# Kernel tuning notes

Hardware: AMD Instinct MI355X
Metric: run time of the kernel (lower is better)

The kernel has to match this reference:

```python
import jax, jax.numpy as jnp
import numpy as np
from math import factorial


def _su2_cg(j1, j2, j3, m1, m2, m3):
    # Complex SU(2) Clebsch-Gordan coefficient <j1 m1; j2 m2 | j3 m3> (Condon-Shortley),
    # same formula as e3nn's _su2_clebsch_gordan_coeff.
    if m3 != m1 + m2:
        return 0.0
    f = factorial
    vmin = max(-j1 + j2 + m3, -j1 + m1, 0)
    vmax = min(j2 + j3 + m1, j3 - j1 + j2, j3 + m3)
    C = ((2 * j3 + 1) * f(j3 + j1 - j2) * f(j3 - j1 + j2) * f(j1 + j2 - j3) / f(j1 + j2 + j3 + 1)
         * f(j3 + m3) * f(j3 - m3) / (f(j1 - m1) * f(j1 + m1) * f(j2 - m2) * f(j2 + m2))) ** 0.5
    S = 0.0
    for v in range(vmin, vmax + 1):
        S += (-1.0) ** (v + j2 + m2) / f(v) * f(j2 + j3 + m1 - v) * f(j1 - m1 + v) / (
            f(j3 - j1 + j2 - v) * f(j3 + m3 - v) * f(v + j1 - j2 - m3))
    return C * S


def _q(l):
    # Change of basis real -> complex spherical harmonics (e3nn convention).
    q = np.zeros((2 * l + 1, 2 * l + 1), dtype=np.complex128)
    for m in range(-l, 0):
        q[l + m, l + abs(m)] = 1 / 2 ** 0.5
        q[l + m, l - abs(m)] = -1j / 2 ** 0.5
    q[l, l] = 1
    for m in range(1, l + 1):
        q[l + m, l + abs(m)] = (-1) ** m / 2 ** 0.5
        q[l + m, l - abs(m)] = 1j * (-1) ** m / 2 ** 0.5
    return (-1j) ** l * q


def _w3j(l1, l2, l3):
    # Real Wigner-3j-like invariant tensor, Frobenius norm 1 (e3nn wigner_3j).
    C = np.zeros((2 * l1 + 1, 2 * l2 + 1, 2 * l3 + 1), dtype=np.complex128)
    for m1 in range(-l1, l1 + 1):
        for m2 in range(-l2, l2 + 1):
            m3 = m1 + m2
            if -l3 <= m3 <= l3:
                C[l1 + m1, l2 + m2, l3 + m3] = _su2_cg(l1, l2, l3, m1, m2, m3)
    C = np.einsum('ij,kl,mn,ikn->jlm', _q(l1), _q(l2), np.conj(_q(l3).T), C)
    C = np.real(C)
    return C / np.linalg.norm(C)


def _cg_full():
    # 1o x 1o -> 0e + 1e + 2e. e3nn FullTensorProduct ('uuu', component norm,
    # element path norm, mul=1) gives path_weight = sqrt(2*l_out + 1) per path.
    return np.concatenate([(2 * l + 1) ** 0.5 * _w3j(1, 1, l) for l in range(3)],
                          axis=-1).astype(np.float32)  # [3, 3, 9]


def setup_inputs() -> dict:
    key = jax.random.key(0)
    N = 8388608  # 2**23 rows, ~96 MB input
    frac = jax.random.normal(key, (N, 3), dtype=jnp.float32)
    cg = jnp.asarray(_cg_full())  # [3, 3, 9] fixed Clebsch-Gordan constants
    return {"frac": frac, "cg": cg}


def reference(frac, cg):
    # SimpleTP.forward: tp(frac, frac) -> [N, 9], then sum over dim 0 -> [9].
    # Fused segment-wise CG contraction + batch reduction in one einsum.
    return jnp.einsum('ni,nj,ijk->k', frac, frac, cg)
```

## Files before the change

### kernel.cpp

```cpp
#include <hip/hip_runtime.h>


constexpr int BLK  = 256;
constexpr int GRID = 2048;

#define ACC6(x, y, z)                                              \
    do {                                                           \
        s00 = fmaf((x), (x), s00); s01 = fmaf((x), (y), s01);      \
        s02 = fmaf((x), (z), s02); s11 = fmaf((y), (y), s11);      \
        s12 = fmaf((y), (z), s12); s22 = fmaf((z), (z), s22);      \
    } while (0)

__global__ __launch_bounds__(BLK) void tp_partial(const float* __restrict__ frac,
                                                  float* __restrict__ ws,
                                                  int nrows) {
    const float4* __restrict__ f4 = reinterpret_cast<const float4*>(frac);
    const int noct   = nrows >> 3;
    const int tid    = blockIdx.x * BLK + threadIdx.x;
    const int stride = GRID * BLK;

    float s00 = 0.f, s01 = 0.f, s02 = 0.f, s11 = 0.f, s12 = 0.f, s22 = 0.f;

    #pragma unroll 2
    for (int g = tid; g < noct; g += stride) {
        const float4* __restrict__ p = f4 + 6L * g;
        float4 v0 = p[0], v1 = p[1], v2 = p[2];
        float4 v3 = p[3], v4 = p[4], v5 = p[5];
        ACC6(v0.x, v0.y, v0.z);
        ACC6(v0.w, v1.x, v1.y);
        ACC6(v1.z, v1.w, v2.x);
        ACC6(v2.y, v2.z, v2.w);
        ACC6(v3.x, v3.y, v3.z);
        ACC6(v3.w, v4.x, v4.y);
        ACC6(v4.z, v4.w, v5.x);
        ACC6(v5.y, v5.z, v5.w);
    }

    if (blockIdx.x == 0 && threadIdx.x == 0) {
        for (int r = (noct << 3); r < nrows; ++r) {
            float x = frac[3L * r + 0], y = frac[3L * r + 1], z = frac[3L * r + 2];
            ACC6(x, y, z);
        }
    }

    #pragma unroll
    for (int off = 32; off > 0; off >>= 1) {
        s00 += __shfl_down(s00, off);
        s01 += __shfl_down(s01, off);
        s02 += __shfl_down(s02, off);
        s11 += __shfl_down(s11, off);
        s12 += __shfl_down(s12, off);
        s22 += __shfl_down(s22, off);
    }

    __shared__ float red[BLK / 64][6];
    const int lane = threadIdx.x & 63;
    const int wave = threadIdx.x >> 6;
    if (lane == 0) {
        red[wave][0] = s00; red[wave][1] = s01; red[wave][2] = s02;
        red[wave][3] = s11; red[wave][4] = s12; red[wave][5] = s22;
    }
    __syncthreads();
    if (threadIdx.x < 6) {
        float v = red[0][threadIdx.x] + red[1][threadIdx.x]
                + red[2][threadIdx.x] + red[3][threadIdx.x];
        ws[threadIdx.x * GRID + blockIdx.x] = v;
    }
}

__global__ __launch_bounds__(BLK) void tp_final(const float* __restrict__ ws,
                                                const float* __restrict__ cg,
                                                float* __restrict__ out) {
    const float4* __restrict__ w4 = reinterpret_cast<const float4*>(ws);
    constexpr int Q = GRID / 4;

    float s[6];
    #pragma unroll
    for (int c = 0; c < 6; ++c) {
        float4 a = w4[c * Q + threadIdx.x];
        float4 b = w4[c * Q + threadIdx.x + BLK];
        s[c] = ((a.x + a.y) + (a.z + a.w)) + ((b.x + b.y) + (b.z + b.w));
    }

    #pragma unroll
    for (int off = 32; off > 0; off >>= 1) {
        #pragma unroll
        for (int c = 0; c < 6; ++c) s[c] += __shfl_down(s[c], off);
    }

    __shared__ float red[BLK / 64][6];
    const int lane = threadIdx.x & 63;
    const int wave = threadIdx.x >> 6;
    if (lane == 0) {
        #pragma unroll
        for (int c = 0; c < 6; ++c) red[wave][c] = s[c];
    }
    __syncthreads();

    __shared__ float M[9];
    if (threadIdx.x == 0) {
        float t[6];
        #pragma unroll
        for (int c = 0; c < 6; ++c)
            t[c] = red[0][c] + red[1][c] + red[2][c] + red[3][c];
        M[0] = t[0];  M[1] = t[1];  M[2] = t[2];
        M[3] = t[1];  M[4] = t[3];  M[5] = t[4];
        M[6] = t[2];  M[7] = t[4];  M[8] = t[5];
    }
    __syncthreads();

    if (threadIdx.x < 9) {
        const int k = threadIdx.x;
        float acc = 0.f;
        #pragma unroll
        for (int p = 0; p < 9; ++p)
            acc = fmaf(M[p], cg[p * 9 + k], acc);
        out[k] = acc;
    }
}

extern "C" void kernel_launch(void* const* d_in, const int* in_sizes, int n_in,
                              void* d_out, int out_size, void* d_ws, size_t ws_size,
                              hipStream_t stream) {
    const float* frac = (const float*)d_in[0];
    const float* cg   = (const float*)d_in[1];
    float*       out  = (float*)d_out;
    float*       ws   = (float*)d_ws;

    const int nrows = in_sizes[0] / 3;

    tp_partial<<<GRID, BLK, 0, stream>>>(frac, ws, nrows);
    tp_final<<<1, BLK, 0, stream>>>(ws, cg, out);
}
```

Baseline: 23.30 us.

## Read input as float4 quads with 2-float lookahead and phase-rotated accumulators

Each thread now reads one float4 per iteration plus the next two floats, instead of six float4s per 8-row octet. The grid is 2046 blocks, a multiple of 3, so the stride in floats is divisible by 3 and each thread's row phase (tid mod 3) stays fixed. The nine phase-relative accumulators are mapped back to the six second moments once at the end. This gives every lane a fully coalesced 16-byte load per step and fewer live registers, at the cost of redundant overlapping 8-byte loads and a padded workspace that needs extra zero writes.

```diff
diff --git a/kernel.cpp b/kernel.cpp
--- a/kernel.cpp
+++ b/kernel.cpp
@@ -2,46 +2,46 @@
 
 
 constexpr int BLK  = 256;
-constexpr int GRID = 2048;
-
-#define ACC6(x, y, z)                                              \
-    do {                                                           \
-        s00 = fmaf((x), (x), s00); s01 = fmaf((x), (y), s01);      \
-        s02 = fmaf((x), (z), s02); s11 = fmaf((y), (y), s11);      \
-        s12 = fmaf((y), (z), s12); s22 = fmaf((z), (z), s22);      \
-    } while (0)
+constexpr int GRID = 2046;
+constexpr int PG   = 2048;
 
 __global__ __launch_bounds__(BLK) void tp_partial(const float* __restrict__ frac,
                                                   float* __restrict__ ws,
-                                                  int nrows) {
+                                                  int nq) {
     const float4* __restrict__ f4 = reinterpret_cast<const float4*>(frac);
-    const int noct   = nrows >> 3;
     const int tid    = blockIdx.x * BLK + threadIdx.x;
     const int stride = GRID * BLK;
 
-    float s00 = 0.f, s01 = 0.f, s02 = 0.f, s11 = 0.f, s12 = 0.f, s22 = 0.f;
+    float r0 = 0.f, r1 = 0.f, r2 = 0.f;
+    float p0 = 0.f, p1 = 0.f, p2 = 0.f;
+    float k0 = 0.f, k1 = 0.f, k2 = 0.f;
 
+    const int full = nq / stride;
+    int g = tid;
     #pragma unroll 2
-    for (int g = tid; g < noct; g += stride) {
-        const float4* __restrict__ p = f4 + 6L * g;
-        float4 v0 = p[0], v1 = p[1], v2 = p[2];
-        float4 v3 = p[3], v4 = p[4], v5 = p[5];
-        ACC6(v0.x, v0.y, v0.z);
-        ACC6(v0.w, v1.x, v1.y);
-        ACC6(v1.z, v1.w, v2.x);
-        ACC6(v2.y, v2.z, v2.w);
-        ACC6(v3.x, v3.y, v3.z);
-        ACC6(v3.w, v4.x, v4.y);
-        ACC6(v4.z, v4.w, v5.x);
-        ACC6(v5.y, v5.z, v5.w);
+    for (int it = 0; it <= full; ++it, g += stride) {
+        if (it == full && g >= nq) break;
+        float4 v = f4[g];
+        float2 e;
+        if (g == nq - 1) e = make_float2(0.f, 0.f);
+        else e = *reinterpret_cast<const float2*>(&frac[4 * g + 4]);
+        const float h0 = v.x, h1 = v.y, h2 = v.z, h3 = v.w, h4 = e.x, h5 = e.y;
+        r0 = fmaf(h0, h0, r0); r0 = fmaf(h3, h3, r0);
+        r1 = fmaf(h1, h1, r1);
+        r2 = fmaf(h2, h2, r2);
+        p0 = fmaf(h0, h1, p0); p0 = fmaf(h3, h4, p0);
+        p1 = fmaf(h1, h2, p1);
+        p2 = fmaf(h2, h3, p2);
+        k0 = fmaf(h0, h2, k0); k0 = fmaf(h3, h5, k0);
+        k1 = fmaf(h1, h3, k1);
+        k2 = fmaf(h2, h4, k2);
     }
 
-    if (blockIdx.x == 0 && threadIdx.x == 0) {
-        for (int r = (noct << 3); r < nrows; ++r) {
-            float x = frac[3L * r + 0], y = frac[3L * r + 1], z = frac[3L * r + 2];
-            ACC6(x, y, z);
-        }
-    }
+    float s00, s01, s02, s11, s12, s22;
+    const int ph = tid % 3;
+    if (ph == 0)      { s00 = r0; s11 = r1; s22 = r2; s01 = p0; s12 = p1; s02 = k0; }
+    else if (ph == 1) { s11 = r0; s22 = r1; s00 = r2; s12 = p0; s01 = p2; s02 = k2; }
+    else              { s22 = r0; s00 = r1; s11 = r2; s01 = p1; s12 = p2; s02 = k1; }
 
     #pragma unroll
     for (int off = 32; off > 0; off >>= 1) {
@@ -64,15 +64,17 @@
     if (threadIdx.x < 6) {
         float v = red[0][threadIdx.x] + red[1][threadIdx.x]
                 + red[2][threadIdx.x] + red[3][threadIdx.x];
-        ws[threadIdx.x * GRID + blockIdx.x] = v;
+        ws[threadIdx.x * PG + blockIdx.x] = v;
     }
+    if (blockIdx.x < PG - GRID && threadIdx.x < 6)
+        ws[threadIdx.x * PG + GRID + blockIdx.x] = 0.f;
 }
 
 __global__ __launch_bounds__(BLK) void tp_final(const float* __restrict__ ws,
                                                 const float* __restrict__ cg,
                                                 float* __restrict__ out) {
     const float4* __restrict__ w4 = reinterpret_cast<const float4*>(ws);
-    constexpr int Q = GRID / 4;
+    constexpr int Q = PG / 4;
 
     float s[6];
     #pragma unroll
@@ -127,8 +129,9 @@
     float*       out  = (float*)d_out;
     float*       ws   = (float*)d_ws;
 
-    const int nrows = in_sizes[0] / 3;
+    const int nfloats = in_sizes[0];
+    const int nq      = nfloats >> 2;
 
-    tp_partial<<<GRID, BLK, 0, stream>>>(frac, ws, nrows);
+    tp_partial<<<GRID, BLK, 0, stream>>>(frac, ws, nq);
     tp_final<<<1, BLK, 0, stream>>>(ws, cg, out);
 }
```

After: 25.80 us. +10.7%, slower.
